# Kernel tuning notes

Measured on AMD Instinct MI355X. Metric: run time of the kernel, lower is better.

## Reference

```python
import math
import jax, jax.numpy as jnp
import numpy as np

N_NODES = 50000
N_EDGES = 600000
IN_CH = 64      # in_channels == out_channels (residual requires it)
HEADS = 2
C = 64          # per-head dim == out_channels
HC = HEADS * C  # 128
EDGE_DIM = 32


def setup_inputs() -> dict:
    key = jax.random.key(0)
    ks = jax.random.split(key, 12)
    s = 0.05
    return {
        "x": jax.random.normal(ks[0], (N_NODES, IN_CH), jnp.float32),
        "edge_index": jax.random.randint(ks[1], (2, N_EDGES), 0, N_NODES, dtype=jnp.int64),
        "edge_attr": jax.random.normal(ks[2], (N_EDGES, EDGE_DIM), jnp.float32),
        "Wq": s * jax.random.normal(ks[3], (IN_CH, HC), jnp.float32),
        "bq": jnp.zeros((HC,), jnp.float32),
        "Wk": s * jax.random.normal(ks[4], (IN_CH, HC), jnp.float32),
        "bk": jnp.zeros((HC,), jnp.float32),
        "Wv": s * jax.random.normal(ks[5], (IN_CH, HC), jnp.float32),
        "bv": jnp.zeros((HC,), jnp.float32),
        "We": s * jax.random.normal(ks[6], (EDGE_DIM, HC), jnp.float32),
        "Wp": s * jax.random.normal(ks[7], (HC, IN_CH), jnp.float32),
        "bp": jnp.zeros((IN_CH,), jnp.float32),
        "ln1_g": jnp.ones((IN_CH,), jnp.float32),
        "ln1_b": jnp.zeros((IN_CH,), jnp.float32),
        "ln2_g": jnp.ones((IN_CH,), jnp.float32),
        "ln2_b": jnp.zeros((IN_CH,), jnp.float32),
        "W1": s * jax.random.normal(ks[8], (IN_CH, IN_CH), jnp.float32),
        "b1": jnp.zeros((IN_CH,), jnp.float32),
        "W2": s * jax.random.normal(ks[9], (IN_CH, IN_CH), jnp.float32),
        "b2": jnp.zeros((IN_CH,), jnp.float32),
    }


def _layernorm(x, g, b, eps=1e-5):
    m = jnp.mean(x, axis=-1, keepdims=True)
    v = jnp.mean(jnp.square(x - m), axis=-1, keepdims=True)
    return (x - m) / jnp.sqrt(v + eps) * g + b


def reference(x, edge_index, edge_attr, Wq, bq, Wk, bk, Wv, bv, We, Wp, bp,
              ln1_g, ln1_b, ln2_g, ln2_b, W1, b1, W2, b2):
    n = x.shape[0]
    residual = x
    h = _layernorm(x, ln1_g, ln1_b)
    q = (h @ Wq + bq).reshape(n, HEADS, C)
    k = (h @ Wk + bk).reshape(n, HEADS, C)
    v = (h @ Wv + bv).reshape(n, HEADS, C)

    src, tgt = edge_index[0], edge_index[1]
    e = (edge_attr @ We).reshape(-1, HEADS, C)   # (E,H,C)
    qi = q[tgt]                                  # (E,H,C) gather by target
    kj = k[src] + e
    vj = v[src] + e

    alpha = jnp.sum(qi * kj, axis=-1) / math.sqrt(C)            # (E,H)
    amax = jax.ops.segment_max(alpha, tgt, num_segments=n)      # (N,H)
    ex = jnp.exp(alpha - amax[tgt])
    den = jax.ops.segment_sum(ex, tgt, num_segments=n)          # (N,H)
    a = ex / (den[tgt] + 1e-8)                                  # (E,H)

    agg = jax.ops.segment_sum(a[:, :, None] * vj, tgt, num_segments=n)  # (N,H,C)
    out = agg.reshape(n, HC) @ Wp + bp
    out = out + residual                        # in_channels == out_channels

    res2 = out
    o = _layernorm(out, ln2_g, ln2_b)
    o = jax.nn.gelu(o @ W1 + b1, approximate=False) @ W2 + b2
    return o + res2
```

## Files before the change

### kernel.cpp

```cpp
#include <hip/hip_runtime.h>
#include <math.h>
#include <stdint.h>


typedef float f32x4 __attribute__((ext_vector_type(4)));
typedef __bf16 bf16x8 __attribute__((ext_vector_type(8)));
typedef unsigned int u32x4 __attribute__((ext_vector_type(4)));

#define WPM_S 200
#define W1_OFF 12800
#define W2_OFF 18432
#define W_TOT 24064
#define H_S 72
#define WC_S 72
#define WC_TOT (448 * 72)
#define QSCALE 0.18033688011112042f

__device__ __forceinline__ unsigned pack_bf16(float2 v) {
    unsigned a = __builtin_bit_cast(unsigned, v.x);
    unsigned b = __builtin_bit_cast(unsigned, v.y);
    a = (a + 0x7FFFu + ((a >> 16) & 1u)) >> 16;
    b = (b + 0x7FFFu + ((b >> 16) & 1u)) >> 16;
    return a | (b << 16);
}
__device__ __forceinline__ float2 unpack_bf16(unsigned p) {
    float x = __builtin_bit_cast(float, p << 16);
    float y = __builtin_bit_cast(float, p & 0xFFFF0000u);
    return make_float2(x, y);
}
__device__ __forceinline__ unsigned short bf16r(float x) {
    unsigned u = __builtin_bit_cast(unsigned, x);
    return (unsigned short)((u + 0x7FFFu + ((u >> 16) & 1u)) >> 16);
}

__device__ __forceinline__ f32x4 mfma16(bf16x8 a, bf16x8 b, f32x4 c) {
    return __builtin_amdgcn_mfma_f32_16x16x32_bf16(a, b, c, 0, 0, 0);
}
__device__ __forceinline__ bf16x8 frag_ld(const unsigned short* p) {
    return __builtin_bit_cast(bf16x8, *(const u32x4*)p);
}

__global__ void k_pre(const float* __restrict__ Wq, const float* __restrict__ Wk,
                      const float* __restrict__ Wv, const float* __restrict__ We,
                      const float* __restrict__ Wp, const float* __restrict__ W1,
                      const float* __restrict__ W2, const float* __restrict__ bq,
                      const float* __restrict__ bk, const float* __restrict__ bv,
                      unsigned short* __restrict__ wsW,
                      unsigned short* __restrict__ wcat, float* __restrict__ bcat,
                      int* __restrict__ deg, int n) {
    int idx = blockIdx.x * 256 + threadIdx.x;
    for (int i = idx; i < n; i += gridDim.x * 256) deg[i] = 0;
    if (idx < 8192) {
        int o = idx >> 7, k = idx & 127;
        wsW[o * WPM_S + k] = bf16r(Wp[((k & 1) * 64 + (k >> 1)) * 64 + o]);
        int cin = idx >> 7, j = idx & 127;
        wcat[j * WC_S + cin] = bf16r(Wq[cin * 128 + j]);
        wcat[(128 + j) * WC_S + cin] = bf16r(Wk[cin * 128 + j]);
        wcat[(256 + j) * WC_S + cin] = bf16r(Wv[cin * 128 + j]);
    }
    if (idx < 4096) {
        int o = idx >> 6, k = idx & 63;
        wsW[W1_OFF + o * 88 + k] = bf16r(W1[k * 64 + o]);
        wsW[W2_OFF + o * 88 + k] = bf16r(W2[k * 64 + o]);
        int o2 = idx & 63, dh = idx >> 6, d = dh >> 1, h = dh & 1;
        float s = 0.f;
        for (int c = 0; c < 64; ++c)
            s += We[d * 128 + h * 64 + c] * Wp[(h * 64 + c) * 64 + o2];
        wsW[o2 * WPM_S + 128 + dh] = bf16r(s);
        int cin2 = idx & 63, dh2 = idx >> 6, d2 = dh2 >> 1, h2 = dh2 & 1;
        float s2 = 0.f;
        for (int c = 0; c < 64; ++c)
            s2 += Wq[cin2 * 128 + h2 * 64 + c] * We[d2 * 128 + h2 * 64 + c];
        wcat[(384 + dh2) * WC_S + cin2] = bf16r(s2);
    }
    if (idx < 384)
        bcat[idx] = idx < 128 ? bq[idx] : idx < 256 ? bk[idx - 128] : bv[idx - 256];
    if (idx < 64) {
        int d = idx >> 1, h = idx & 1;
        float s = 0.f;
        for (int c = 0; c < 64; ++c)
            s += bq[h * 64 + c] * We[d * 128 + h * 64 + c];
        bcat[384 + idx] = s;
    }
}

__global__ __launch_bounds__(256) void k_bucket(
    const int* __restrict__ ei, int* __restrict__ deg,
    int* __restrict__ bucket_e, unsigned short* __restrict__ bucket_s,
    int E, int n) {
    int e = blockIdx.x * 256 + threadIdx.x;
    if (e >= E) return;
    int src = ei[e], tgt = ei[E + e];
    src = min(max(src, 0), n - 1);
    tgt = min(max(tgt, 0), n - 1);
    int slot = atomicAdd(&deg[tgt], 1);
    if (slot < 64) {
        bucket_e[(size_t)tgt * 64 + slot] = e;
        bucket_s[(size_t)tgt * 64 + slot] = (unsigned short)src;
    }
}

__global__ __launch_bounds__(256) void k_qkv(
    const float* __restrict__ x, const unsigned short* __restrict__ wcat,
    const float* __restrict__ bcat,
    const float* __restrict__ g1, const float* __restrict__ b1,
    unsigned* __restrict__ qx, unsigned* __restrict__ kbf,
    unsigned* __restrict__ vbf, int n) {
    __shared__ __align__(16) unsigned short sW[WC_TOT];
    int tid = threadIdx.x;
    for (int i = tid; i < WC_TOT / 8; i += 256)
        ((u32x4*)sW)[i] = ((const u32x4*)wcat)[i];
    __syncthreads();

    int wave = tid >> 6, lane = tid & 63;
    int cl = lane & 15, kg = lane >> 4;
    int node0 = blockIdx.x * 64 + wave * 16;
    if (node0 >= n) return;
    int arow = min(node0 + cl, n - 1);

    const float4* xp = (const float4*)(x + (size_t)arow * 64);
    float4 xv[4] = {xp[kg * 2], xp[kg * 2 + 1], xp[8 + kg * 2], xp[9 + kg * 2]};
    float s1 = 0.f, s2 = 0.f;
#pragma unroll
    for (int i = 0; i < 4; ++i) {
        s1 += (xv[i].x + xv[i].y) + (xv[i].z + xv[i].w);
        s2 += xv[i].x * xv[i].x + xv[i].y * xv[i].y
            + xv[i].z * xv[i].z + xv[i].w * xv[i].w;
    }
    s1 += __shfl_xor(s1, 16); s2 += __shfl_xor(s2, 16);
    s1 += __shfl_xor(s1, 32); s2 += __shfl_xor(s2, 32);
    float mean = s1 * 0.015625f;
    float var  = s2 * 0.015625f - mean * mean;
    float rstd = rsqrtf(var + 1e-5f);
    const float4* gp = (const float4*)g1;
    const float4* bp1 = (const float4*)b1;
    float4 gv[4] = {gp[kg * 2], gp[kg * 2 + 1], gp[8 + kg * 2], gp[9 + kg * 2]};
    float4 bv4[4] = {bp1[kg * 2], bp1[kg * 2 + 1], bp1[8 + kg * 2], bp1[9 + kg * 2]};
    unsigned fr[8];
#pragma unroll
    for (int i = 0; i < 4; ++i) {
        float h0 = (xv[i].x - mean) * rstd * gv[i].x + bv4[i].x;
        float h1 = (xv[i].y - mean) * rstd * gv[i].y + bv4[i].y;
        float h2 = (xv[i].z - mean) * rstd * gv[i].z + bv4[i].z;
        float h3 = (xv[i].w - mean) * rstd * gv[i].w + bv4[i].w;
        fr[i * 2]     = pack_bf16(make_float2(h0, h1));
        fr[i * 2 + 1] = pack_bf16(make_float2(h2, h3));
    }
    bf16x8 A0 = __builtin_bit_cast(bf16x8, (u32x4){fr[0], fr[1], fr[2], fr[3]});
    bf16x8 A1 = __builtin_bit_cast(bf16x8, (u32x4){fr[4], fr[5], fr[6], fr[7]});

#pragma unroll
    for (int tq = 0; tq < 4; ++tq) {
        int c = tq * 16 + cl;
        f32x4 aq0 = {bcat[c], bcat[c], bcat[c], bcat[c]};
        float b_;
        b_ = bcat[64 + c];  f32x4 aq1 = {b_, b_, b_, b_};
        b_ = bcat[128 + c]; f32x4 ak0 = {b_, b_, b_, b_};
        b_ = bcat[192 + c]; f32x4 ak1 = {b_, b_, b_, b_};
        b_ = bcat[256 + c]; f32x4 av0 = {b_, b_, b_, b_};
        b_ = bcat[320 + c]; f32x4 av1 = {b_, b_, b_, b_};
        b_ = bcat[384 + c]; f32x4 aw  = {b_, b_, b_, b_};
#pragma unroll
        for (int s = 0; s < 2; ++s) {
            bf16x8 A = s ? A1 : A0;
            int ko = s * 32 + kg * 8;
            aq0 = mfma16(A, frag_ld(sW + (size_t)(c) * WC_S + ko), aq0);
            aq1 = mfma16(A, frag_ld(sW + (size_t)(64 + c) * WC_S + ko), aq1);
            ak0 = mfma16(A, frag_ld(sW + (size_t)(128 + c) * WC_S + ko), ak0);
            ak1 = mfma16(A, frag_ld(sW + (size_t)(192 + c) * WC_S + ko), ak1);
            av0 = mfma16(A, frag_ld(sW + (size_t)(256 + c) * WC_S + ko), av0);
            av1 = mfma16(A, frag_ld(sW + (size_t)(320 + c) * WC_S + ko), av1);
            aw  = mfma16(A, frag_ld(sW + (size_t)(384 + c) * WC_S + ko), aw);
        }
#pragma unroll
        for (int j = 0; j < 4; ++j) {
            int node = node0 + kg * 4 + j;
            if (node < n) {
                qx[(size_t)node * 128 + c] =
                    pack_bf16(make_float2(aq0[j] * QSCALE, aq1[j] * QSCALE));
                kbf[(size_t)node * 64 + c] = pack_bf16(make_float2(ak0[j], ak1[j]));
                vbf[(size_t)node * 64 + c] = pack_bf16(make_float2(av0[j], av1[j]));
                ((float*)qx)[(size_t)node * 128 + 64 + c] = aw[j] * QSCALE;
            }
        }
    }
}

__global__ __launch_bounds__(256) void k_attn(
    const unsigned* __restrict__ qx, const unsigned* __restrict__ kbf,
    const unsigned* __restrict__ vbf, const float* __restrict__ edge_attr,
    const int* __restrict__ deg, const int* __restrict__ bucket_e,
    const unsigned short* __restrict__ bucket_s,
    unsigned* __restrict__ aggs, int n, int E) {
    int wave = threadIdx.x >> 6, lane = threadIdx.x & 63;
    int node = blockIdx.x * 4 + wave;
    if (node >= n) return;
    int sub = lane >> 4, l = lane & 15;

    uint4 qq = ((const uint4*)qx)[(size_t)node * 32 + l];
    float4 w4 = ((const float4*)qx)[(size_t)node * 32 + 16 + l];
    float2 q0 = unpack_bf16(qq.x), q1 = unpack_bf16(qq.y),
           q2 = unpack_bf16(qq.z), q3 = unpack_bf16(qq.w);

    int dcount = min(deg[node], 64);
    int eid_l = 0, src_l = 0;
    if (lane < dcount) {
        eid_l = min(max(bucket_e[(size_t)node * 64 + lane], 0), E - 1);
        src_l = min((int)bucket_s[(size_t)node * 64 + lane], n - 1);
    }

    const uint4* kb4 = (const uint4*)kbf;
    const uint4* vb4 = (const uint4*)vbf;
    const float2* ea2 = (const float2*)edge_attr;

    float accA[4] = {0.f, 0.f, 0.f, 0.f}, accB[4] = {0.f, 0.f, 0.f, 0.f};
    float aS0 = 0.f, aS1 = 0.f, bS0 = 0.f, bS1 = 0.f;
    float den0 = 0.f, den1 = 0.f;

    uint4 kk, vv; float2 a2;
    {
        int jj = sub & 63;
        int ej = __shfl(eid_l, jj), sj = __shfl(src_l, jj);
        kk = kb4[(size_t)sj * 16 + l];
        vv = vb4[(size_t)sj * 16 + l];
        a2 = ea2[(size_t)ej * 16 + l];
    }
    for (int i = 0; i < dcount; i += 4) {
        uint4 kc = kk, vc = vv; float2 ac = a2;
        bool valid = (i + sub) < dcount;
        int inx = i + 4;
        if (inx < dcount) {
            int jj = (inx + sub) & 63;
            int ej = __shfl(eid_l, jj), sj = __shfl(src_l, jj);
            kk = kb4[(size_t)sj * 16 + l];
            vv = vb4[(size_t)sj * 16 + l];
            a2 = ea2[(size_t)ej * 16 + l];
        }
        float2 k0 = unpack_bf16(kc.x), k1 = unpack_bf16(kc.y),
               k2 = unpack_bf16(kc.z), k3 = unpack_bf16(kc.w);
        float r0 = q0.x * k0.x + q1.x * k1.x + q2.x * k2.x + q3.x * k3.x
                 + w4.x * ac.x + w4.z * ac.y;
        float r1 = q0.y * k0.y + q1.y * k1.y + q2.y * k2.y + q3.y * k3.y
                 + w4.y * ac.x + w4.w * ac.y;
#pragma unroll
        for (int m = 1; m < 16; m <<= 1) {
            r0 += __shfl_xor(r0, m);
            r1 += __shfl_xor(r1, m);
        }
        float ex0 = valid ? exp2f(r0) : 0.f;
        float ex1 = valid ? exp2f(r1) : 0.f;
        float2 v0 = unpack_bf16(vc.x), v1 = unpack_bf16(vc.y),
               v2 = unpack_bf16(vc.z), v3 = unpack_bf16(vc.w);
        accA[0] += ex0 * v0.x; accB[0] += ex1 * v0.y;
        accA[1] += ex0 * v1.x; accB[1] += ex1 * v1.y;
        accA[2] += ex0 * v2.x; accB[2] += ex1 * v2.y;
        accA[3] += ex0 * v3.x; accB[3] += ex1 * v3.y;
        aS0 += ex0 * ac.x; aS1 += ex1 * ac.x;
        bS0 += ex0 * ac.y; bS1 += ex1 * ac.y;
        den0 += ex0; den1 += ex1;
    }

#pragma unroll
    for (int m = 16; m < 64; m <<= 1) {
#pragma unroll
        for (int j = 0; j < 4; ++j) {
            accA[j] += __shfl_xor(accA[j], m);
            accB[j] += __shfl_xor(accB[j], m);
        }
        aS0 += __shfl_xor(aS0, m); aS1 += __shfl_xor(aS1, m);
        bS0 += __shfl_xor(bS0, m); bS1 += __shfl_xor(bS1, m);
        den0 += __shfl_xor(den0, m); den1 += __shfl_xor(den1, m);
    }

    float r0 = 1.0f / (den0 + 1e-8f);
    float r1 = 1.0f / (den1 + 1e-8f);

    float va = sub == 0 ? accA[0] : sub == 1 ? accA[1]
             : sub == 2 ? accA[2] : accA[3];
    float vb = sub == 0 ? accB[0] : sub == 1 ? accB[1]
             : sub == 2 ? accB[2] : accB[3];
    aggs[(size_t)node * 96 + 4 * l + sub] =
        pack_bf16(make_float2(va * r0, vb * r1));

    if (sub == 0) {
        unsigned s0 = pack_bf16(make_float2(aS0 * r0, aS1 * r1));
        unsigned s1 = pack_bf16(make_float2(bS0 * r0, bS1 * r1));
        *(uint2*)&aggs[(size_t)node * 96 + 64 + 2 * l] = make_uint2(s0, s1);
    }
}

__global__ __launch_bounds__(256) void k_post(
    const unsigned short* __restrict__ aggsb,
    const unsigned short* __restrict__ wsW,
    const float* __restrict__ bp, const float* __restrict__ x,
    const float* __restrict__ g2, const float* __restrict__ b2,
    const float* __restrict__ b1f, const float* __restrict__ b2f,
    float* __restrict__ out, int n) {
    __shared__ __align__(16) unsigned short sW[W_TOT];
    __shared__ __align__(16) unsigned short hb[4][2][16 * H_S];
    int tid = threadIdx.x;
    for (int i = tid; i < W_TOT / 8; i += 256)
        ((u32x4*)sW)[i] = ((const u32x4*)wsW)[i];
    __syncthreads();

    int wave = tid >> 6, lane = tid & 63;
    int cl = lane & 15, kg = lane >> 4;
    unsigned short* h2 = hb[wave][0];
    unsigned short* h3 = hb[wave][1];

    float bp_c[4], g2_c[4], b2_c[4], b1_c[4], bf2_c[4];
#pragma unroll
    for (int t = 0; t < 4; ++t) {
        int c = t * 16 + cl;
        bp_c[t] = bp[c];
        g2_c[t] = g2[c];
        b2_c[t] = b2[c];
        b1_c[t] = b1f[c];
        bf2_c[t] = b2f[c];
    }

    int wid = blockIdx.x * 4 + wave;
    int nbatch = (n + 15) >> 4;
    int nwaves = gridDim.x * 4;
    for (int bt = wid; bt < nbatch; bt += nwaves) {
        int node0 = bt * 16;

        f32x4 acc1[4];
#pragma unroll
        for (int t = 0; t < 4; ++t) acc1[t] = (f32x4){0.f, 0.f, 0.f, 0.f};
        int arow = min(node0 + cl, n - 1);
#pragma unroll
        for (int s = 0; s < 6; ++s) {
            bf16x8 af = frag_ld(aggsb + (size_t)arow * 192 + s * 32 + kg * 8);
#pragma unroll
            for (int t = 0; t < 4; ++t) {
                bf16x8 bf = frag_ld(sW + (t * 16 + cl) * WPM_S + s * 32 + kg * 8);
                acc1[t] = mfma16(af, bf, acc1[t]);
            }
        }
#pragma unroll
        for (int t = 0; t < 4; ++t) {
#pragma unroll
            for (int j = 0; j < 4; ++j) {
                int nd = min(node0 + kg * 4 + j, n - 1);
                acc1[t][j] += bp_c[t] + x[(size_t)nd * 64 + t * 16 + cl];
            }
        }

        float mean[4], rstd[4];
#pragma unroll
        for (int j = 0; j < 4; ++j) {
            float s1 = acc1[0][j] + acc1[1][j] + acc1[2][j] + acc1[3][j];
            float s2 = acc1[0][j] * acc1[0][j] + acc1[1][j] * acc1[1][j]
                     + acc1[2][j] * acc1[2][j] + acc1[3][j] * acc1[3][j];
#pragma unroll
            for (int m = 1; m < 16; m <<= 1) {
                s1 += __shfl_xor(s1, m);
                s2 += __shfl_xor(s2, m);
            }
            mean[j] = s1 * 0.015625f;
            float var = s2 * 0.015625f - mean[j] * mean[j];
            rstd[j] = rsqrtf(var + 1e-5f);
        }
#pragma unroll
        for (int t = 0; t < 4; ++t)
#pragma unroll
            for (int j = 0; j < 4; ++j) {
                float v = (acc1[t][j] - mean[j]) * rstd[j] * g2_c[t] + b2_c[t];
                h2[(kg * 4 + j) * H_S + t * 16 + cl] = bf16r(v);
            }
        asm volatile("s_waitcnt lgkmcnt(0)" ::: "memory");

        f32x4 acc2[4];
#pragma unroll
        for (int t = 0; t < 4; ++t)
            acc2[t] = (f32x4){b1_c[t], b1_c[t], b1_c[t], b1_c[t]};
#pragma unroll
        for (int s = 0; s < 2; ++s) {
            bf16x8 af = frag_ld(h2 + cl * H_S + s * 32 + kg * 8);
#pragma unroll
            for (int t = 0; t < 4; ++t) {
                bf16x8 bf = frag_ld(sW + W1_OFF + (t * 16 + cl) * 88 + s * 32 + kg * 8);
                acc2[t] = mfma16(af, bf, acc2[t]);
            }
        }
#pragma unroll
        for (int t = 0; t < 4; ++t)
#pragma unroll
            for (int j = 0; j < 4; ++j) {
                float v = acc2[t][j];
                v = 0.5f * v * (1.0f + erff(v * 0.70710678118654752f));
                h3[(kg * 4 + j) * H_S + t * 16 + cl] = bf16r(v);
            }
        asm volatile("s_waitcnt lgkmcnt(0)" ::: "memory");

        f32x4 acc3[4];
#pragma unroll
        for (int t = 0; t < 4; ++t) {
            acc3[t] = acc1[t];
#pragma unroll
            for (int j = 0; j < 4; ++j) acc3[t][j] += bf2_c[t];
        }
#pragma unroll
        for (int s = 0; s < 2; ++s) {
            bf16x8 af = frag_ld(h3 + cl * H_S + s * 32 + kg * 8);
#pragma unroll
            for (int t = 0; t < 4; ++t) {
                bf16x8 bf = frag_ld(sW + W2_OFF + (t * 16 + cl) * 88 + s * 32 + kg * 8);
                acc3[t] = mfma16(af, bf, acc3[t]);
            }
        }
#pragma unroll
        for (int t = 0; t < 4; ++t)
#pragma unroll
            for (int j = 0; j < 4; ++j) {
                int r = node0 + kg * 4 + j;
                if (r < n) out[(size_t)r * 64 + t * 16 + cl] = acc3[t][j];
            }
    }
}

extern "C" void kernel_launch(void* const* d_in, const int* in_sizes, int n_in,
                              void* d_out, int out_size, void* d_ws, size_t ws_size,
                              hipStream_t stream) {
    const float* x  = (const float*)d_in[0];
    const int*   ei = (const int*)d_in[1];
    const float* ea = (const float*)d_in[2];
    const float* Wq = (const float*)d_in[3];
    const float* bq = (const float*)d_in[4];
    const float* Wk = (const float*)d_in[5];
    const float* bk = (const float*)d_in[6];
    const float* Wv = (const float*)d_in[7];
    const float* bv = (const float*)d_in[8];
    const float* We = (const float*)d_in[9];
    const float* Wp = (const float*)d_in[10];
    const float* bp = (const float*)d_in[11];
    const float* g1 = (const float*)d_in[12];
    const float* b1 = (const float*)d_in[13];
    const float* g2 = (const float*)d_in[14];
    const float* b2 = (const float*)d_in[15];
    const float* W1 = (const float*)d_in[16];
    const float* b1f = (const float*)d_in[17];
    const float* W2 = (const float*)d_in[18];
    const float* b2f = (const float*)d_in[19];

    const int n = in_sizes[0] / 64;
    const int E = in_sizes[2] / 32;

    char* p = (char*)d_ws;
    unsigned* qx = (unsigned*)p; p += (size_t)n * 128 * 4;
    unsigned* kbf = (unsigned*)p; p += (size_t)n * 64 * 4;
    unsigned* vbf = (unsigned*)p; p += (size_t)n * 64 * 4;
    int* deg   = (int*)p;   p += (size_t)n * 4;
    p = (char*)(((uintptr_t)p + 15) & ~(uintptr_t)15);
    int* bucket_e = (int*)p; p += (size_t)n * 64 * 4;
    unsigned short* bucket_s = (unsigned short*)p; p += (size_t)n * 64 * 2;
    p = (char*)(((uintptr_t)p + 15) & ~(uintptr_t)15);
    unsigned* aggs = (unsigned*)p; p += (size_t)n * 96 * 4;
    unsigned short* wsW = (unsigned short*)p; p += W_TOT * 2;
    unsigned short* wcat = (unsigned short*)p; p += (size_t)WC_TOT * 2;
    float* bcat = (float*)p; p += 448 * 4;

    k_pre<<<196, 256, 0, stream>>>(Wq, Wk, Wv, We, Wp, W1, W2, bq, bk, bv,
                                   wsW, wcat, bcat, deg, n);
    k_bucket<<<(E + 255) / 256, 256, 0, stream>>>(ei, deg, bucket_e, bucket_s,
                                                  E, n);
    k_qkv<<<(n + 63) / 64, 256, 0, stream>>>(x, wcat, bcat, g1, b1,
                                             qx, kbf, vbf, n);
    k_attn<<<(n + 3) / 4, 256, 0, stream>>>(qx, kbf, vbf, ea, deg,
                                            bucket_e, bucket_s, aggs, n, E);
    int nb16 = (n + 15) >> 4;
    int blocks = (nb16 + 3) / 4;
    if (blocks > 391) blocks = 391;
    k_post<<<blocks, 256, 0, stream>>>((const unsigned short*)aggs, wsW,
                                       bp, x, g2, b2, b1f, b2f,
                                       (float*)d_out, n);
}
```

Measured before the change: 295.6 us.

## Process two target nodes per wave in attention, double qkv block size

The attention kernel now has each wave handle two target nodes, interleaving their gather loads and softmax-aggregation so more independent memory requests are in flight per wave. This is meant to hide gather latency. The cost is roughly double the register use, which can lower occupancy, plus wasted iterations when the two nodes' degrees differ. Separately, the QKV projection kernel moves from 256-thread to 512-thread blocks (128 nodes each), so the shared-memory weight load is amortised over more nodes.

After: 296.1 us. Within noise of the previous version (+0.2%).

```diff
diff --git a/kernel.cpp b/kernel.cpp
--- a/kernel.cpp
+++ b/kernel.cpp
@@ -100,7 +100,7 @@
     }
 }
 
-__global__ __launch_bounds__(256) void k_qkv(
+__global__ __launch_bounds__(512) void k_qkv(
     const float* __restrict__ x, const unsigned short* __restrict__ wcat,
     const float* __restrict__ bcat,
     const float* __restrict__ g1, const float* __restrict__ b1,
@@ -108,13 +108,13 @@
     unsigned* __restrict__ vbf, int n) {
     __shared__ __align__(16) unsigned short sW[WC_TOT];
     int tid = threadIdx.x;
-    for (int i = tid; i < WC_TOT / 8; i += 256)
+    for (int i = tid; i < WC_TOT / 8; i += 512)
         ((u32x4*)sW)[i] = ((const u32x4*)wcat)[i];
     __syncthreads();
 
     int wave = tid >> 6, lane = tid & 63;
     int cl = lane & 15, kg = lane >> 4;
-    int node0 = blockIdx.x * 64 + wave * 16;
+    int node0 = blockIdx.x * 128 + wave * 16;
     if (node0 >= n) return;
     int arow = min(node0 + cl, n - 1);
 
@@ -193,99 +193,173 @@
     const unsigned short* __restrict__ bucket_s,
     unsigned* __restrict__ aggs, int n, int E) {
     int wave = threadIdx.x >> 6, lane = threadIdx.x & 63;
-    int node = blockIdx.x * 4 + wave;
-    if (node >= n) return;
+    int nodeA = (blockIdx.x * 4 + wave) * 2;
+    if (nodeA >= n) return;
+    int nodeB = nodeA + 1;
+    bool hasB = nodeB < n;
+    int nB = hasB ? nodeB : nodeA;
     int sub = lane >> 4, l = lane & 15;
 
-    uint4 qq = ((const uint4*)qx)[(size_t)node * 32 + l];
-    float4 w4 = ((const float4*)qx)[(size_t)node * 32 + 16 + l];
-    float2 q0 = unpack_bf16(qq.x), q1 = unpack_bf16(qq.y),
-           q2 = unpack_bf16(qq.z), q3 = unpack_bf16(qq.w);
-
-    int dcount = min(deg[node], 64);
-    int eid_l = 0, src_l = 0;
-    if (lane < dcount) {
-        eid_l = min(max(bucket_e[(size_t)node * 64 + lane], 0), E - 1);
-        src_l = min((int)bucket_s[(size_t)node * 64 + lane], n - 1);
+    uint4 qqA = ((const uint4*)qx)[(size_t)nodeA * 32 + l];
+    float4 w4A = ((const float4*)qx)[(size_t)nodeA * 32 + 16 + l];
+    uint4 qqB = ((const uint4*)qx)[(size_t)nB * 32 + l];
+    float4 w4B = ((const float4*)qx)[(size_t)nB * 32 + 16 + l];
+    float2 qA0 = unpack_bf16(qqA.x), qA1 = unpack_bf16(qqA.y),
+           qA2 = unpack_bf16(qqA.z), qA3 = unpack_bf16(qqA.w);
+    float2 qB0 = unpack_bf16(qqB.x), qB1 = unpack_bf16(qqB.y),
+           qB2 = unpack_bf16(qqB.z), qB3 = unpack_bf16(qqB.w);
+
+    int dA = min(deg[nodeA], 64);
+    int dB = hasB ? min(deg[nodeB], 64) : 0;
+    int eidA = 0, srcA = 0, eidB = 0, srcB = 0;
+    if (lane < dA) {
+        eidA = min(max(bucket_e[(size_t)nodeA * 64 + lane], 0), E - 1);
+        srcA = min((int)bucket_s[(size_t)nodeA * 64 + lane], n - 1);
+    }
+    if (lane < dB) {
+        eidB = min(max(bucket_e[(size_t)nB * 64 + lane], 0), E - 1);
+        srcB = min((int)bucket_s[(size_t)nB * 64 + lane], n - 1);
     }
 
     const uint4* kb4 = (const uint4*)kbf;
     const uint4* vb4 = (const uint4*)vbf;
     const float2* ea2 = (const float2*)edge_attr;
 
-    float accA[4] = {0.f, 0.f, 0.f, 0.f}, accB[4] = {0.f, 0.f, 0.f, 0.f};
-    float aS0 = 0.f, aS1 = 0.f, bS0 = 0.f, bS1 = 0.f;
-    float den0 = 0.f, den1 = 0.f;
-
-    uint4 kk, vv; float2 a2;
+    float aAh0[4] = {0.f, 0.f, 0.f, 0.f}, aAh1[4] = {0.f, 0.f, 0.f, 0.f};
+    float aBh0[4] = {0.f, 0.f, 0.f, 0.f}, aBh1[4] = {0.f, 0.f, 0.f, 0.f};
+    float SA0a = 0.f, SA0b = 0.f, SA1a = 0.f, SA1b = 0.f;
+    float SB0a = 0.f, SB0b = 0.f, SB1a = 0.f, SB1b = 0.f;
+    float dnA0 = 0.f, dnA1 = 0.f, dnB0 = 0.f, dnB1 = 0.f;
+
+    uint4 kkA, vvA, kkB, vvB; float2 aaA, aaB;
     {
-        int jj = sub & 63;
-        int ej = __shfl(eid_l, jj), sj = __shfl(src_l, jj);
-        kk = kb4[(size_t)sj * 16 + l];
-        vv = vb4[(size_t)sj * 16 + l];
-        a2 = ea2[(size_t)ej * 16 + l];
-    }
-    for (int i = 0; i < dcount; i += 4) {
-        uint4 kc = kk, vc = vv; float2 ac = a2;
-        bool valid = (i + sub) < dcount;
+        int jj = sub;
+        int ej = __shfl(eidA, jj), sj = __shfl(srcA, jj);
+        kkA = kb4[(size_t)sj * 16 + l];
+        vvA = vb4[(size_t)sj * 16 + l];
+        aaA = ea2[(size_t)ej * 16 + l];
+        ej = __shfl(eidB, jj); sj = __shfl(srcB, jj);
+        kkB = kb4[(size_t)sj * 16 + l];
+        vvB = vb4[(size_t)sj * 16 + l];
+        aaB = ea2[(size_t)ej * 16 + l];
+    }
+    int dmax = max(dA, dB);
+    for (int i = 0; i < dmax; i += 4) {
+        uint4 kcA = kkA, vcA = vvA; float2 acA = aaA;
+        uint4 kcB = kkB, vcB = vvB; float2 acB = aaB;
         int inx = i + 4;
-        if (inx < dcount) {
+        if (inx < dA) {
             int jj = (inx + sub) & 63;
-            int ej = __shfl(eid_l, jj), sj = __shfl(src_l, jj);
-            kk = kb4[(size_t)sj * 16 + l];
-            vv = vb4[(size_t)sj * 16 + l];
-            a2 = ea2[(size_t)ej * 16 + l];
-        }
-        float2 k0 = unpack_bf16(kc.x), k1 = unpack_bf16(kc.y),
-               k2 = unpack_bf16(kc.z), k3 = unpack_bf16(kc.w);
-        float r0 = q0.x * k0.x + q1.x * k1.x + q2.x * k2.x + q3.x * k3.x
-                 + w4.x * ac.x + w4.z * ac.y;
-        float r1 = q0.y * k0.y + q1.y * k1.y + q2.y * k2.y + q3.y * k3.y
-                 + w4.y * ac.x + w4.w * ac.y;
-#pragma unroll
-        for (int m = 1; m < 16; m <<= 1) {
-            r0 += __shfl_xor(r0, m);
-            r1 += __shfl_xor(r1, m);
-        }
-        float ex0 = valid ? exp2f(r0) : 0.f;
-        float ex1 = valid ? exp2f(r1) : 0.f;
-        float2 v0 = unpack_bf16(vc.x), v1 = unpack_bf16(vc.y),
-               v2 = unpack_bf16(vc.z), v3 = unpack_bf16(vc.w);
-        accA[0] += ex0 * v0.x; accB[0] += ex1 * v0.y;
-        accA[1] += ex0 * v1.x; accB[1] += ex1 * v1.y;
-        accA[2] += ex0 * v2.x; accB[2] += ex1 * v2.y;
-        accA[3] += ex0 * v3.x; accB[3] += ex1 * v3.y;
-        aS0 += ex0 * ac.x; aS1 += ex1 * ac.x;
-        bS0 += ex0 * ac.y; bS1 += ex1 * ac.y;
-        den0 += ex0; den1 += ex1;
+            int ej = __shfl(eidA, jj), sj = __shfl(srcA, jj);
+            kkA = kb4[(size_t)sj * 16 + l];
+            vvA = vb4[(size_t)sj * 16 + l];
+            aaA = ea2[(size_t)ej * 16 + l];
+        }
+        if (inx < dB) {
+            int jj = (inx + sub) & 63;
+            int ej = __shfl(eidB, jj), sj = __shfl(srcB, jj);
+            kkB = kb4[(size_t)sj * 16 + l];
+            vvB = vb4[(size_t)sj * 16 + l];
+            aaB = ea2[(size_t)ej * 16 + l];
+        }
+        if (i < dA) {
+            float2 k0 = unpack_bf16(kcA.x), k1 = unpack_bf16(kcA.y),
+                   k2 = unpack_bf16(kcA.z), k3 = unpack_bf16(kcA.w);
+            float r0 = qA0.x * k0.x + qA1.x * k1.x + qA2.x * k2.x + qA3.x * k3.x
+                     + w4A.x * acA.x + w4A.z * acA.y;
+            float r1 = qA0.y * k0.y + qA1.y * k1.y + qA2.y * k2.y + qA3.y * k3.y
+                     + w4A.y * acA.x + w4A.w * acA.y;
+#pragma unroll
+            for (int m = 1; m < 16; m <<= 1) {
+                r0 += __shfl_xor(r0, m);
+                r1 += __shfl_xor(r1, m);
+            }
+            bool valid = (i + sub) < dA;
+            float ex0 = valid ? exp2f(r0) : 0.f;
+            float ex1 = valid ? exp2f(r1) : 0.f;
+            float2 v0 = unpack_bf16(vcA.x), v1 = unpack_bf16(vcA.y),
+                   v2 = unpack_bf16(vcA.z), v3 = unpack_bf16(vcA.w);
+            aAh0[0] += ex0 * v0.x; aAh1[0] += ex1 * v0.y;
+            aAh0[1] += ex0 * v1.x; aAh1[1] += ex1 * v1.y;
+            aAh0[2] += ex0 * v2.x; aAh1[2] += ex1 * v2.y;
+            aAh0[3] += ex0 * v3.x; aAh1[3] += ex1 * v3.y;
+            SA0a += ex0 * acA.x; SA0b += ex1 * acA.x;
+            SA1a += ex0 * acA.y; SA1b += ex1 * acA.y;
+            dnA0 += ex0; dnA1 += ex1;
+        }
+        if (i < dB) {
+            float2 k0 = unpack_bf16(kcB.x), k1 = unpack_bf16(kcB.y),
+                   k2 = unpack_bf16(kcB.z), k3 = unpack_bf16(kcB.w);
+            float r0 = qB0.x * k0.x + qB1.x * k1.x + qB2.x * k2.x + qB3.x * k3.x
+                     + w4B.x * acB.x + w4B.z * acB.y;
+            float r1 = qB0.y * k0.y + qB1.y * k1.y + qB2.y * k2.y + qB3.y * k3.y
+                     + w4B.y * acB.x + w4B.w * acB.y;
+#pragma unroll
+            for (int m = 1; m < 16; m <<= 1) {
+                r0 += __shfl_xor(r0, m);
+                r1 += __shfl_xor(r1, m);
+            }
+            bool valid = (i + sub) < dB;
+            float ex0 = valid ? exp2f(r0) : 0.f;
+            float ex1 = valid ? exp2f(r1) : 0.f;
+            float2 v0 = unpack_bf16(vcB.x), v1 = unpack_bf16(vcB.y),
+                   v2 = unpack_bf16(vcB.z), v3 = unpack_bf16(vcB.w);
+            aBh0[0] += ex0 * v0.x; aBh1[0] += ex1 * v0.y;
+            aBh0[1] += ex0 * v1.x; aBh1[1] += ex1 * v1.y;
+            aBh0[2] += ex0 * v2.x; aBh1[2] += ex1 * v2.y;
+            aBh0[3] += ex0 * v3.x; aBh1[3] += ex1 * v3.y;
+            SB0a += ex0 * acB.x; SB0b += ex1 * acB.x;
+            SB1a += ex0 * acB.y; SB1b += ex1 * acB.y;
+            dnB0 += ex0; dnB1 += ex1;
+        }
     }
 
 #pragma unroll
     for (int m = 16; m < 64; m <<= 1) {
 #pragma unroll
         for (int j = 0; j < 4; ++j) {
-            accA[j] += __shfl_xor(accA[j], m);
-            accB[j] += __shfl_xor(accB[j], m);
-        }
-        aS0 += __shfl_xor(aS0, m); aS1 += __shfl_xor(aS1, m);
-        bS0 += __shfl_xor(bS0, m); bS1 += __shfl_xor(bS1, m);
-        den0 += __shfl_xor(den0, m); den1 += __shfl_xor(den1, m);
-    }
-
-    float r0 = 1.0f / (den0 + 1e-8f);
-    float r1 = 1.0f / (den1 + 1e-8f);
-
-    float va = sub == 0 ? accA[0] : sub == 1 ? accA[1]
-             : sub == 2 ? accA[2] : accA[3];
-    float vb = sub == 0 ? accB[0] : sub == 1 ? accB[1]
-             : sub == 2 ? accB[2] : accB[3];
-    aggs[(size_t)node * 96 + 4 * l + sub] =
-        pack_bf16(make_float2(va * r0, vb * r1));
-
-    if (sub == 0) {
-        unsigned s0 = pack_bf16(make_float2(aS0 * r0, aS1 * r1));
-        unsigned s1 = pack_bf16(make_float2(bS0 * r0, bS1 * r1));
-        *(uint2*)&aggs[(size_t)node * 96 + 64 + 2 * l] = make_uint2(s0, s1);
+            aAh0[j] += __shfl_xor(aAh0[j], m);
+            aAh1[j] += __shfl_xor(aAh1[j], m);
+            aBh0[j] += __shfl_xor(aBh0[j], m);
+            aBh1[j] += __shfl_xor(aBh1[j], m);
+        }
+        SA0a += __shfl_xor(SA0a, m); SA0b += __shfl_xor(SA0b, m);
+        SA1a += __shfl_xor(SA1a, m); SA1b += __shfl_xor(SA1b, m);
+        SB0a += __shfl_xor(SB0a, m); SB0b += __shfl_xor(SB0b, m);
+        SB1a += __shfl_xor(SB1a, m); SB1b += __shfl_xor(SB1b, m);
+        dnA0 += __shfl_xor(dnA0, m); dnA1 += __shfl_xor(dnA1, m);
+        dnB0 += __shfl_xor(dnB0, m); dnB1 += __shfl_xor(dnB1, m);
+    }
+
+    {
+        float r0 = 1.0f / (dnA0 + 1e-8f);
+        float r1 = 1.0f / (dnA1 + 1e-8f);
+        float va = sub == 0 ? aAh0[0] : sub == 1 ? aAh0[1]
+                 : sub == 2 ? aAh0[2] : aAh0[3];
+        float vb = sub == 0 ? aAh1[0] : sub == 1 ? aAh1[1]
+                 : sub == 2 ? aAh1[2] : aAh1[3];
+        aggs[(size_t)nodeA * 96 + 4 * l + sub] =
+            pack_bf16(make_float2(va * r0, vb * r1));
+        if (sub == 0) {
+            unsigned s0 = pack_bf16(make_float2(SA0a * r0, SA0b * r1));
+            unsigned s1 = pack_bf16(make_float2(SA1a * r0, SA1b * r1));
+            *(uint2*)&aggs[(size_t)nodeA * 96 + 64 + 2 * l] = make_uint2(s0, s1);
+        }
+    }
+    if (hasB) {
+        float r0 = 1.0f / (dnB0 + 1e-8f);
+        float r1 = 1.0f / (dnB1 + 1e-8f);
+        float va = sub == 0 ? aBh0[0] : sub == 1 ? aBh0[1]
+                 : sub == 2 ? aBh0[2] : aBh0[3];
+        float vb = sub == 0 ? aBh1[0] : sub == 1 ? aBh1[1]
+                 : sub == 2 ? aBh1[2] : aBh1[3];
+        aggs[(size_t)nodeB * 96 + 4 * l + sub] =
+            pack_bf16(make_float2(va * r0, vb * r1));
+        if (sub == 0) {
+            unsigned s0 = pack_bf16(make_float2(SB0a * r0, SB0b * r1));
+            unsigned s1 = pack_bf16(make_float2(SB1a * r0, SB1b * r1));
+            *(uint2*)&aggs[(size_t)nodeB * 96 + 64 + 2 * l] = make_uint2(s0, s1);
+        }
     }
 }
 
@@ -465,10 +539,11 @@
                                    wsW, wcat, bcat, deg, n);
     k_bucket<<<(E + 255) / 256, 256, 0, stream>>>(ei, deg, bucket_e, bucket_s,
                                                   E, n);
-    k_qkv<<<(n + 63) / 64, 256, 0, stream>>>(x, wcat, bcat, g1, b1,
-                                             qx, kbf, vbf, n);
-    k_attn<<<(n + 3) / 4, 256, 0, stream>>>(qx, kbf, vbf, ea, deg,
-                                            bucket_e, bucket_s, aggs, n, E);
+    k_qkv<<<(n + 127) / 128, 512, 0, stream>>>(x, wcat, bcat, g1, b1,
+                                               qx, kbf, vbf, n);
+    int pairs = (n + 1) / 2;
+    k_attn<<<(pairs + 3) / 4, 256, 0, stream>>>(qx, kbf, vbf, ea, deg,
+                                                bucket_e, bucket_s, aggs, n, E);
     int nb16 = (n + 15) >> 4;
     int blocks = (nb16 + 3) / 4;
     if (blocks > 391) blocks = 391;
```
